# Performance work log

Hardware: AMD Instinct MI355X
Metric: run time of the kernel (lower is better)

## Reference

```python
import jax, jax.numpy as jnp
import numpy as np

B, E, H, W = 8, 16, 512, 512
K = 32  # max instance ids (labels in 1..K; 0 = background)
DELTA_VAR, DELTA_DIST = 0.5, 1.5
ALPHA, BETA, GAMMA = 1.0, 1.0, 0.001


def setup_inputs() -> dict:
    key = jax.random.key(0)
    k1, k2 = jax.random.split(key)
    embedding = jax.random.normal(k1, (B, E, H, W), dtype=jnp.float32)
    instance_mask = jax.random.randint(k2, (B, H, W), 0, K + 1, dtype=jnp.int32)
    return {"embedding": embedding, "instance_mask": instance_mask}


def reference(embedding, instance_mask):
    b, e, h, w = embedding.shape
    n = h * w
    emb = embedding.reshape(b, e, n)                 # [B,E,N]
    mask = instance_mask.reshape(b, n)               # [B,N]
    dt = emb.dtype

    # one-hot instance membership [B,K,N]
    onehot = (mask[:, None, :] == jnp.arange(1, K + 1, dtype=mask.dtype)[None, :, None]).astype(dt)
    counts = onehot.sum(-1)                          # [B,K]
    present = counts > 0                             # [B,K]
    presentf = present.astype(dt)
    safe_counts = jnp.maximum(counts, 1.0)

    # instance centers (masked means) [B,K,E]
    centers = jnp.einsum('ben,bkn->bke', emb, onehot) / safe_counts[..., None]

    # ---- variance term: per-pixel distance to own instance center ----
    labels = jnp.maximum(mask - 1, 0)                # bg -> arbitrary index 0 (masked out)
    center_px = jnp.take_along_axis(centers, labels[:, :, None], axis=1)  # [B,N,E]
    fg = (mask > 0).astype(dt)
    sq = ((jnp.swapaxes(emb, 1, 2) - center_px) ** 2).sum(-1)             # [B,N]
    d = jnp.sqrt(jnp.where(mask > 0, sq, 1.0))
    hinged2 = jnp.maximum(d - DELTA_VAR, 0.0) ** 2 * fg                   # [B,N]
    per_inst = jnp.einsum('bn,bkn->bk', hinged2, onehot) / safe_counts    # per-instance mean
    n_inst = presentf.sum(-1)                        # [B]
    valid = n_inst > 0
    safe_n = jnp.maximum(n_inst, 1.0)
    loss_var_b = per_inst.sum(-1) / safe_n

    # ---- distance term: hinged pairwise center distances (i<j, both present) ----
    iu = jnp.arange(K)
    pair_mask = present[:, :, None] & present[:, None, :] & (iu[:, None] < iu[None, :])
    dsq = ((centers[:, :, None, :] - centers[:, None, :, :]) ** 2).sum(-1)  # [B,K,K]
    dd = jnp.sqrt(jnp.where(pair_mask, dsq, 1.0))
    hp = jnp.maximum(2.0 * DELTA_DIST - dd, 0.0) ** 2 * pair_mask.astype(dt)
    n_pairs = n_inst * (n_inst - 1.0) * 0.5
    loss_dist_b = hp.sum((1, 2)) / jnp.maximum(n_pairs, 1.0)

    # ---- regularization term: mean norm of present centers ----
    csq = (centers ** 2).sum(-1)                     # [B,K]
    cn = jnp.sqrt(jnp.where(present, csq, 1.0)) * presentf
    loss_reg_b = cn.sum(-1) / safe_n

    # ---- mean over valid batches ----
    validf = valid.astype(dt)
    vb = jnp.maximum(validf.sum(), 1.0)
    L_var = (loss_var_b * validf).sum() / vb
    L_dist = (loss_dist_b * validf).sum() / vb
    L_reg = (loss_reg_b * validf).sum() / vb
    total = ALPHA * L_var + BETA * L_dist + GAMMA * L_reg
    return total, L_var, L_dist, L_reg
```

## Files before the change

### kernel.cpp

```cpp
#include <hip/hip_runtime.h>
#include <hip/hip_bf16.h>

#define BB 8
#define EE 16
#define NN 262144
#define KK 32
#define DELTA_VAR 0.5f
#define TWO_DELTA_DIST 3.0f
#define GAMMA_REG 0.001f

#define P1 1024
#define P3 1024

#define SCALE_S 262144.0f
#define SCALE_V 1024.0f


__global__ __launch_bounds__(256) void k1_sums(const float* __restrict__ emb,
                                               const int* __restrict__ mask,
                                               unsigned long long* __restrict__ q_sums,
                                               unsigned int* __restrict__ q_cnt) {
    __shared__ int hist[EE * 33];
    __shared__ unsigned int chist[KK];
    const int t = threadIdx.x;
    const int b = blockIdx.y;

    for (int i = t; i < EE * 33; i += 256) hist[i] = 0;
    if (t < KK) chist[t] = 0u;
    __syncthreads();

    const int n0 = blockIdx.x * P1;
    const int fidx = (n0 >> 2) + t;

    const float4* ef = (const float4*)(emb + (size_t)b * EE * NN);
    float4 x[EE];
    #pragma unroll
    for (int e = 0; e < EE; e++) x[e] = ef[(size_t)e * (NN / 4) + fidx];
    int4 l4 = ((const int4*)(mask + (size_t)b * NN + n0))[t];
    int ks[4] = {l4.x, l4.y, l4.z, l4.w};

    #pragma unroll
    for (int j = 0; j < 4; j++) {
        int k = ks[j];
        if (k > 0) {
            int kk = k - 1;
            atomicAdd(&chist[kk], 1u);
            #pragma unroll
            for (int e = 0; e < EE; e++) {
                float xv = (j == 0) ? x[e].x : (j == 1) ? x[e].y
                         : (j == 2) ? x[e].z : x[e].w;
                atomicAdd(&hist[e * 33 + kk], (int)rintf(xv * SCALE_S));
            }
        }
    }
    __syncthreads();

    for (int idx = t; idx < KK * EE; idx += 256) {
        int ee = idx >> 5, k = idx & 31;
        long long val = (long long)hist[ee * 33 + k];
        atomicAdd(&q_sums[((size_t)b * KK + k) * EE + ee],
                  (unsigned long long)val);
    }
    if (t < KK) atomicAdd(&q_cnt[b * KK + t], chist[t]);
}

__global__ __launch_bounds__(256) void k2_centers(const unsigned long long* __restrict__ q_sums,
                                                  const unsigned int* __restrict__ q_cnt,
                                                  float* __restrict__ g_cen,
                                                  float* __restrict__ g_cntf) {
    const int t = threadIdx.x;
    for (int idx = t; idx < BB * KK * EE; idx += 256) {
        int bk = idx >> 4;
        float cnt = (float)q_cnt[bk];
        float s = (float)(long long)q_sums[idx] * (1.0f / SCALE_S);
        g_cen[idx] = s / fmaxf(cnt, 1.0f);
    }
    for (int bk = t; bk < BB * KK; bk += 256) g_cntf[bk] = (float)q_cnt[bk];
}

__global__ __launch_bounds__(256) void k3_var(const float* __restrict__ emb,
                                              const int* __restrict__ mask,
                                              const float* __restrict__ g_cen,
                                              unsigned long long* __restrict__ q_var) {
    __shared__ float c_lds[KK * 17];
    __shared__ unsigned int vhist[KK];
    const int t = threadIdx.x;
    const int b = blockIdx.y;
    const int n0 = blockIdx.x * P3;

    for (int idx = t; idx < KK * EE; idx += 256) {
        int k = idx >> 4, e = idx & 15;
        c_lds[k * 17 + e] = g_cen[idx + (size_t)b * KK * EE];
    }
    if (t < KK) vhist[t] = 0u;
    __syncthreads();

    const float4* ef = (const float4*)(emb + (size_t)b * EE * NN);
    const int fidx = (n0 >> 2) + t;
    float4 x[EE];
    #pragma unroll
    for (int e = 0; e < EE; e++) x[e] = ef[(size_t)e * (NN / 4) + fidx];
    int4 l4 = ((const int4*)(mask + (size_t)b * NN + n0))[t];
    int ks[4] = {l4.x, l4.y, l4.z, l4.w};

    #pragma unroll
    for (int j = 0; j < 4; j++) {
        int k = ks[j];
        if (k > 0) {
            const float* c = &c_lds[(k - 1) * 17];
            float sq = 0.0f;
            #pragma unroll
            for (int e = 0; e < EE; e++) {
                float xv = (j == 0) ? x[e].x : (j == 1) ? x[e].y
                         : (j == 2) ? x[e].z : x[e].w;
                float d = xv - c[e];
                sq += d * d;
            }
            float dd = sqrtf(sq);
            float h = fmaxf(dd - DELTA_VAR, 0.0f);
            unsigned int q = (unsigned int)rintf(h * h * SCALE_V);
            atomicAdd(&vhist[k - 1], q);
        }
    }
    __syncthreads();

    if (t < KK) atomicAdd(&q_var[b * KK + t], (unsigned long long)vhist[t]);
}

__global__ __launch_bounds__(256) void k4_final(const float* __restrict__ g_cen,
                                                const float* __restrict__ g_cntf,
                                                const unsigned long long* __restrict__ q_var,
                                                float* __restrict__ out) {
    __shared__ float cen[BB][KK][EE];
    __shared__ float pres[BB][KK];
    __shared__ float red[BB][4];
    const int t = threadIdx.x;
    const int b = t >> 5, k = t & 31;

    float cnt = g_cntf[b * KK + k];
    float sc = fmaxf(cnt, 1.0f);
    float c2 = 0.0f;
    #pragma unroll
    for (int e = 0; e < EE; e++) {
        float c = g_cen[((size_t)b * KK + k) * EE + e];
        cen[b][k][e] = c;
        c2 += c * c;
    }
    float presf = (cnt > 0.0f) ? 1.0f : 0.0f;
    pres[b][k] = presf;
    float per_inst = (float)((double)q_var[b * KK + k] * (1.0 / SCALE_V)) / sc;
    float cn = presf * sqrtf(c2);
    __syncthreads();

    float hp = 0.0f;
    if (presf > 0.0f) {
        for (int j = k + 1; j < KK; j++) {
            if (pres[b][j] > 0.0f) {
                float dsq = 0.0f;
                #pragma unroll
                for (int e = 0; e < EE; e++) {
                    float d = cen[b][k][e] - cen[b][j][e];
                    dsq += d * d;
                }
                float dd = sqrtf(dsq);
                float h = fmaxf(TWO_DELTA_DIST - dd, 0.0f);
                hp += h * h;
            }
        }
    }

    float v0 = per_inst, v1 = hp, v2 = cn, v3 = presf;
    #pragma unroll
    for (int off = 16; off > 0; off >>= 1) {
        v0 += __shfl_down(v0, off, 32);
        v1 += __shfl_down(v1, off, 32);
        v2 += __shfl_down(v2, off, 32);
        v3 += __shfl_down(v3, off, 32);
    }
    if (k == 0) {
        float n_inst = v3;
        float validf = (n_inst > 0.0f) ? 1.0f : 0.0f;
        float safe_n = fmaxf(n_inst, 1.0f);
        float lv = v0 / safe_n;
        float npairs = n_inst * (n_inst - 1.0f) * 0.5f;
        float ld = v1 / fmaxf(npairs, 1.0f);
        float lr = v2 / safe_n;
        red[b][0] = lv * validf;
        red[b][1] = ld * validf;
        red[b][2] = lr * validf;
        red[b][3] = validf;
    }
    __syncthreads();
    if (t == 0) {
        float sv = 0, sd = 0, sr = 0, vb = 0;
        for (int b2 = 0; b2 < BB; b2++) {
            sv += red[b2][0]; sd += red[b2][1]; sr += red[b2][2]; vb += red[b2][3];
        }
        vb = fmaxf(vb, 1.0f);
        float L_var = sv / vb, L_dist = sd / vb, L_reg = sr / vb;
        out[0] = L_var + L_dist + GAMMA_REG * L_reg;
        out[1] = L_var;
        out[2] = L_dist;
        out[3] = L_reg;
    }
}

extern "C" void kernel_launch(void* const* d_in, const int* in_sizes, int n_in,
                              void* d_out, int out_size, void* d_ws, size_t ws_size,
                              hipStream_t stream) {
    const float* emb  = (const float*)d_in[0];
    const int*   mask = (const int*)d_in[1];
    float* out = (float*)d_out;
    char* ws = (char*)d_ws;

    unsigned long long* q_sums = (unsigned long long*)(ws);
    unsigned int*       q_cnt  = (unsigned int*)(ws + 32768);
    unsigned long long* q_var  = (unsigned long long*)(ws + 33792);
    float*              g_cen  = (float*)(ws + 35840);
    float*              g_cntf = (float*)(ws + 52224);

    hipMemsetAsync(d_ws, 0, 35840, stream);

    dim3 blk(256);
    k1_sums<<<dim3(NN / P1, BB), blk, 0, stream>>>(emb, mask, q_sums, q_cnt);
    k2_centers<<<dim3(1), blk, 0, stream>>>(q_sums, q_cnt, g_cen, g_cntf);
    k3_var<<<dim3(NN / P3, BB), blk, 0, stream>>>(emb, mask, g_cen, q_var);
    k4_final<<<dim3(1), blk, 0, stream>>>(g_cen, g_cntf, q_var, out);
}
```

Baseline: 282.1 us.

## Replace global 64-bit atomics with per-block partials and deterministic reduction kernels

Each k1 block now writes its local histogram row (sums and counts) to a partial buffer instead of doing global 64-bit atomics, and a new multi-block k2_reduce sums the partials. k3 likewise writes per-block variance partials, which k4 reduces. This drops the memset and global atomic contention. k1 also processes 2048 pixels per block, which halves the number of partial rows. The cost is extra partial-buffer traffic and a serial reduction loop inside the single-block final kernel.

```diff
diff --git a/kernel.cpp b/kernel.cpp
--- a/kernel.cpp
+++ b/kernel.cpp
@@ -1,5 +1,4 @@
 #include <hip/hip_runtime.h>
-#include <hip/hip_bf16.h>
 
 #define BB 8
 #define EE 16
@@ -9,98 +8,116 @@
 #define TWO_DELTA_DIST 3.0f
 #define GAMMA_REG 0.001f
 
-#define P1 1024
+#define P1 2048
+#define NBX1 (NN / P1)
 #define P3 1024
+#define NBX3 (NN / P3)
+#define COLS 544
 
 #define SCALE_S 262144.0f
 #define SCALE_V 1024.0f
+#define INV_SS (1.0 / 262144.0)
+#define INV_SV (1.0 / 1024.0)
 
 
 __global__ __launch_bounds__(256) void k1_sums(const float* __restrict__ emb,
                                                const int* __restrict__ mask,
-                                               unsigned long long* __restrict__ q_sums,
-                                               unsigned int* __restrict__ q_cnt) {
+                                               int* __restrict__ P_part) {
     __shared__ int hist[EE * 33];
     __shared__ unsigned int chist[KK];
     const int t = threadIdx.x;
-    const int b = blockIdx.y;
+    const int bx = blockIdx.x, b = blockIdx.y;
 
     for (int i = t; i < EE * 33; i += 256) hist[i] = 0;
     if (t < KK) chist[t] = 0u;
     __syncthreads();
 
-    const int n0 = blockIdx.x * P1;
-    const int fidx = (n0 >> 2) + t;
-
     const float4* ef = (const float4*)(emb + (size_t)b * EE * NN);
-    float4 x[EE];
-    #pragma unroll
-    for (int e = 0; e < EE; e++) x[e] = ef[(size_t)e * (NN / 4) + fidx];
-    int4 l4 = ((const int4*)(mask + (size_t)b * NN + n0))[t];
-    int ks[4] = {l4.x, l4.y, l4.z, l4.w};
-
-    #pragma unroll
-    for (int j = 0; j < 4; j++) {
-        int k = ks[j];
-        if (k > 0) {
-            int kk = k - 1;
-            atomicAdd(&chist[kk], 1u);
-            #pragma unroll
-            for (int e = 0; e < EE; e++) {
-                float xv = (j == 0) ? x[e].x : (j == 1) ? x[e].y
-                         : (j == 2) ? x[e].z : x[e].w;
-                atomicAdd(&hist[e * 33 + kk], (int)rintf(xv * SCALE_S));
+    const int4*   mp = (const int4*)(mask + (size_t)b * NN);
+    const int f0 = bx * (P1 / 4);
+
+    #pragma unroll
+    for (int r = 0; r < P1 / 1024; r++) {
+        const int fidx = f0 + r * 256 + t;
+        float4 x[EE];
+        #pragma unroll
+        for (int e = 0; e < EE; e++) x[e] = ef[(size_t)e * (NN / 4) + fidx];
+        int4 l4 = mp[fidx];
+        int ks[4] = {l4.x, l4.y, l4.z, l4.w};
+
+        #pragma unroll
+        for (int j = 0; j < 4; j++) {
+            int k = ks[j];
+            if (k > 0) {
+                int kk = k - 1;
+                atomicAdd(&chist[kk], 1u);
+                #pragma unroll
+                for (int e = 0; e < EE; e++) {
+                    float xv = (j == 0) ? x[e].x : (j == 1) ? x[e].y
+                             : (j == 2) ? x[e].z : x[e].w;
+                    atomicAdd(&hist[e * 33 + kk], (int)rintf(xv * SCALE_S));
+                }
             }
         }
     }
     __syncthreads();
 
-    for (int idx = t; idx < KK * EE; idx += 256) {
-        int ee = idx >> 5, k = idx & 31;
-        long long val = (long long)hist[ee * 33 + k];
-        atomicAdd(&q_sums[((size_t)b * KK + k) * EE + ee],
-                  (unsigned long long)val);
-    }
-    if (t < KK) atomicAdd(&q_cnt[b * KK + t], chist[t]);
-}
-
-__global__ __launch_bounds__(256) void k2_centers(const unsigned long long* __restrict__ q_sums,
-                                                  const unsigned int* __restrict__ q_cnt,
-                                                  float* __restrict__ g_cen,
-                                                  float* __restrict__ g_cntf) {
-    const int t = threadIdx.x;
-    for (int idx = t; idx < BB * KK * EE; idx += 256) {
-        int bk = idx >> 4;
-        float cnt = (float)q_cnt[bk];
-        float s = (float)(long long)q_sums[idx] * (1.0f / SCALE_S);
-        g_cen[idx] = s / fmaxf(cnt, 1.0f);
-    }
-    for (int bk = t; bk < BB * KK; bk += 256) g_cntf[bk] = (float)q_cnt[bk];
+    int* row = P_part + ((size_t)b * NBX1 + bx) * COLS;
+    for (int c = t; c < COLS; c += 256) {
+        int v = (c < 512) ? hist[(c >> 5) * 33 + (c & 31)] : (int)chist[c - 512];
+        row[c] = v;
+    }
+}
+
+__global__ __launch_bounds__(256) void k2_reduce(const int* __restrict__ P_part,
+                                                 float* __restrict__ g_sumf,
+                                                 float* __restrict__ g_cntf) {
+    __shared__ long long part[4][64];
+    const int t = threadIdx.x;
+    const int g = blockIdx.x, b = blockIdx.y;
+    const int cl = t & 63, rc = t >> 6;
+    const int col = g * 64 + cl;
+
+    long long acc = 0;
+    if (col < COLS) {
+        const int* base = P_part + (size_t)b * NBX1 * COLS + col;
+        #pragma unroll 8
+        for (int r = rc * (NBX1 / 4); r < (rc + 1) * (NBX1 / 4); r++)
+            acc += base[(size_t)r * COLS];
+    }
+    part[rc][cl] = acc;
+    __syncthreads();
+    if (t < 64 && col < COLS) {
+        long long s = part[0][cl] + part[1][cl] + part[2][cl] + part[3][cl];
+        if (col < 512) g_sumf[b * 512 + col] = (float)((double)s * INV_SS);
+        else           g_cntf[b * KK + (col - 512)] = (float)s;
+    }
 }
 
 __global__ __launch_bounds__(256) void k3_var(const float* __restrict__ emb,
                                               const int* __restrict__ mask,
-                                              const float* __restrict__ g_cen,
-                                              unsigned long long* __restrict__ q_var) {
+                                              const float* __restrict__ g_sumf,
+                                              const float* __restrict__ g_cntf,
+                                              unsigned int* __restrict__ v_part) {
     __shared__ float c_lds[KK * 17];
     __shared__ unsigned int vhist[KK];
     const int t = threadIdx.x;
-    const int b = blockIdx.y;
-    const int n0 = blockIdx.x * P3;
-
-    for (int idx = t; idx < KK * EE; idx += 256) {
-        int k = idx >> 4, e = idx & 15;
-        c_lds[k * 17 + e] = g_cen[idx + (size_t)b * KK * EE];
+    const int bx = blockIdx.x, b = blockIdx.y;
+
+    for (int idx = t; idx < 512; idx += 256) {
+        int e = idx >> 5, k = idx & 31;
+        float cnt = g_cntf[b * KK + k];
+        c_lds[k * 17 + e] = g_sumf[b * 512 + idx] / fmaxf(cnt, 1.0f);
     }
     if (t < KK) vhist[t] = 0u;
     __syncthreads();
 
     const float4* ef = (const float4*)(emb + (size_t)b * EE * NN);
-    const int fidx = (n0 >> 2) + t;
+    const int fidx = bx * (P3 / 4) + t;
     float4 x[EE];
     #pragma unroll
     for (int e = 0; e < EE; e++) x[e] = ef[(size_t)e * (NN / 4) + fidx];
-    int4 l4 = ((const int4*)(mask + (size_t)b * NN + n0))[t];
+    int4 l4 = ((const int4*)(mask + (size_t)b * NN))[fidx];
     int ks[4] = {l4.x, l4.y, l4.z, l4.w};
 
     #pragma unroll
@@ -118,18 +135,17 @@
             }
             float dd = sqrtf(sq);
             float h = fmaxf(dd - DELTA_VAR, 0.0f);
-            unsigned int q = (unsigned int)rintf(h * h * SCALE_V);
-            atomicAdd(&vhist[k - 1], q);
-        }
-    }
-    __syncthreads();
-
-    if (t < KK) atomicAdd(&q_var[b * KK + t], (unsigned long long)vhist[t]);
-}
-
-__global__ __launch_bounds__(256) void k4_final(const float* __restrict__ g_cen,
+            atomicAdd(&vhist[k - 1], (unsigned int)rintf(h * h * SCALE_V));
+        }
+    }
+    __syncthreads();
+
+    if (t < KK) v_part[((size_t)b * NBX3 + bx) * KK + t] = vhist[t];
+}
+
+__global__ __launch_bounds__(256) void k4_final(const float* __restrict__ g_sumf,
                                                 const float* __restrict__ g_cntf,
-                                                const unsigned long long* __restrict__ q_var,
+                                                const unsigned int* __restrict__ v_part,
                                                 float* __restrict__ out) {
     __shared__ float cen[BB][KK][EE];
     __shared__ float pres[BB][KK];
@@ -137,18 +153,23 @@
     const int t = threadIdx.x;
     const int b = t >> 5, k = t & 31;
 
+    unsigned long long vacc = 0ull;
+    const unsigned int* vp = v_part + (size_t)b * NBX3 * KK + k;
+    #pragma unroll 8
+    for (int r = 0; r < NBX3; r++) vacc += vp[(size_t)r * KK];
+
     float cnt = g_cntf[b * KK + k];
     float sc = fmaxf(cnt, 1.0f);
     float c2 = 0.0f;
     #pragma unroll
     for (int e = 0; e < EE; e++) {
-        float c = g_cen[((size_t)b * KK + k) * EE + e];
+        float c = g_sumf[b * 512 + e * 32 + k] / sc;
         cen[b][k][e] = c;
         c2 += c * c;
     }
     float presf = (cnt > 0.0f) ? 1.0f : 0.0f;
     pres[b][k] = presf;
-    float per_inst = (float)((double)q_var[b * KK + k] * (1.0 / SCALE_V)) / sc;
+    float per_inst = (float)((double)vacc * INV_SV) / sc;
     float cn = presf * sqrtf(c2);
     __syncthreads();
 
@@ -213,17 +234,14 @@
     float* out = (float*)d_out;
     char* ws = (char*)d_ws;
 
-    unsigned long long* q_sums = (unsigned long long*)(ws);
-    unsigned int*       q_cnt  = (unsigned int*)(ws + 32768);
-    unsigned long long* q_var  = (unsigned long long*)(ws + 33792);
-    float*              g_cen  = (float*)(ws + 35840);
-    float*              g_cntf = (float*)(ws + 52224);
-
-    hipMemsetAsync(d_ws, 0, 35840, stream);
+    int*          P_part = (int*)(ws);
+    unsigned int* v_part = (unsigned int*)(ws + 2228224);
+    float*        g_sumf = (float*)(ws + 2490368);
+    float*        g_cntf = (float*)(ws + 2506752);
 
     dim3 blk(256);
-    k1_sums<<<dim3(NN / P1, BB), blk, 0, stream>>>(emb, mask, q_sums, q_cnt);
-    k2_centers<<<dim3(1), blk, 0, stream>>>(q_sums, q_cnt, g_cen, g_cntf);
-    k3_var<<<dim3(NN / P3, BB), blk, 0, stream>>>(emb, mask, g_cen, q_var);
-    k4_final<<<dim3(1), blk, 0, stream>>>(g_cen, g_cntf, q_var, out);
-}
+    k1_sums <<<dim3(NBX1, BB), blk, 0, stream>>>(emb, mask, P_part);
+    k2_reduce<<<dim3(9,    BB), blk, 0, stream>>>(P_part, g_sumf, g_cntf);
+    k3_var  <<<dim3(NBX3, BB), blk, 0, stream>>>(emb, mask, g_sumf, g_cntf, v_part);
+    k4_final<<<dim3(1),        blk, 0, stream>>>(g_sumf, g_cntf, v_part, out);
+}
```

Result: slower. 291.6 us (+3.4%).
